# Kernel tuning notes

Measured on AMD Instinct MI355X. Metric: run time of the kernel, lower is better.

## Reference

```python
import jax, jax.numpy as jnp
import numpy as np

DIMS = [1024, 2048, 2048, 51]
B, P = 16, 1024


def setup_inputs() -> dict:
    key = jax.random.key(0)
    ks = jax.random.split(key, 1 + 2 * (len(DIMS) - 1))
    inp = {
        "num_pairs": P,
        "classifier_input": jax.random.normal(ks[0], (B, P, DIMS[0]), dtype=jnp.float32),
        "num_batches": B,
    }
    # Linear params, PyTorch-style: W[out, in], b[out]
    for li in range(len(DIMS) - 1):
        fan_in = DIMS[li]
        bound = 1.0 / np.sqrt(fan_in)
        inp[f"W{li}"] = jax.random.uniform(ks[1 + 2 * li], (DIMS[li + 1], fan_in), minval=-bound, maxval=bound, dtype=jnp.float32)
        inp[f"b{li}"] = jax.random.uniform(ks[2 + 2 * li], (DIMS[li + 1],), minval=-bound, maxval=bound, dtype=jnp.float32)
    return inp


def reference(num_pairs, classifier_input, num_batches, W0, b0, W1, b1, W2, b2):
    # Batched MLP over all (num_batches * num_pairs) vectors at once.
    # Original loops per (b, i); math is identical. dropout p=0.0 -> identity.
    x = classifier_input  # [B, P, d_in]
    x = jax.nn.relu(jnp.einsum("bpd,hd->bph", x, W0) + b0)
    x = jax.nn.relu(jnp.einsum("bpd,hd->bph", x, W1) + b1)
    out = jnp.einsum("bpd,od->bpo", x, W2) + b2  # [B, P, n_classes]
    return out
```

## Files before the change

### kernel.cpp

```cpp
#include <hip/hip_runtime.h>
#include <hip/hip_bf16.h>
#include <stdint.h>

typedef __attribute__((ext_vector_type(8))) short short8;
typedef __attribute__((ext_vector_type(8))) uint16_t ushort8;
typedef __attribute__((ext_vector_type(4))) float floatx4;

#define TK 64


__device__ __forceinline__ uint16_t f2bf_bits(float f) {
    uint32_t u = __builtin_bit_cast(uint32_t, f);
    u += 0x7FFFu + ((u >> 16) & 1u);
    return (uint16_t)(u >> 16);
}

__device__ __forceinline__ void async_copy16(const void* g, void* l) {
    auto gp = (const __attribute__((address_space(1))) uint32_t*)(uintptr_t)g;
    auto lp = (__attribute__((address_space(3))) uint32_t*)(uint32_t)(uintptr_t)l;
    __builtin_amdgcn_global_load_lds(gp, lp, 16, 0, 0);
}


__global__ void cvt8(const float* __restrict__ src, uint16_t* __restrict__ dst, int n) {
    int i = (blockIdx.x * 256 + threadIdx.x) * 8;
    if (i >= n) return;
    floatx4 a = *(const floatx4*)(src + i);
    floatx4 b = *(const floatx4*)(src + i + 4);
    ushort8 o;
#pragma unroll
    for (int k = 0; k < 4; k++) {
        o[k]     = f2bf_bits(a[k]);
        o[k + 4] = f2bf_bits(b[k]);
    }
    *(ushort8*)(dst + i) = o;
}

__global__ void cvt_pad_w2(const float* __restrict__ src, uint16_t* __restrict__ dst) {
    int i = (blockIdx.x * 256 + threadIdx.x) * 8;
    int row = i >> 11;
    ushort8 o;
    if (row < 51) {
        floatx4 a = *(const floatx4*)(src + i);
        floatx4 b = *(const floatx4*)(src + i + 4);
#pragma unroll
        for (int k = 0; k < 4; k++) {
            o[k]     = f2bf_bits(a[k]);
            o[k + 4] = f2bf_bits(b[k]);
        }
    } else {
#pragma unroll
        for (int k = 0; k < 8; k++) o[k] = 0;
    }
    *(ushort8*)(dst + i) = o;
}


template <int MI, int NJ, bool RELU, bool OUTF32>
__global__ __launch_bounds__(256, 2)
void gemm_bt(const uint16_t* __restrict__ A,
             const uint16_t* __restrict__ W,
             const float* __restrict__ bias,
             void* __restrict__ out,
             int M, int N, int K, int ldc, int nstore)
{
    constexpr int TMv = MI * 32;
    constexpr int TNv = NJ * 32;
    constexpr int ACH = TMv / 32;
    constexpr int BCH = TNv / 32;

    __shared__ alignas(16) uint16_t sA[TMv * TK];
    __shared__ alignas(16) uint16_t sB[TNv * TK];

    const int tid  = threadIdx.x;
    const int wave = tid >> 6;
    const int lane = tid & 63;

    const int f   = blockIdx.x;
    const int xcd = f & 7;
    const int loc = f >> 3;
    const int per = (int)gridDim.x >> 3;
    const int nt  = N / TNv;
    const int n_t = loc % nt;
    const int m_t = xcd * (per / nt) + loc / nt;
    const int n0 = n_t * TNv;
    const int m0 = m_t * TMv;

    floatx4 acc[MI][NJ];
    const floatx4 zero = {0.f, 0.f, 0.f, 0.f};
#pragma unroll
    for (int i = 0; i < MI; i++)
#pragma unroll
        for (int j = 0; j < NJ; j++) acc[i][j] = zero;

    const int wr = (wave >> 1) * MI * 16;
    const int wc = (wave & 1) * NJ * 16;

    const int sr   = lane >> 3;
    const int scol = ((lane & 7) ^ sr) * 8;

    const uint16_t* ap[ACH];
    const uint16_t* bp[BCH];
#pragma unroll
    for (int t = 0; t < ACH; t++)
        ap[t] = A + (size_t)(m0 + (wave + 4 * t) * 8 + sr) * K + scol;
#pragma unroll
    for (int t = 0; t < BCH; t++)
        bp[t] = W + (size_t)(n0 + (wave + 4 * t) * 8 + sr) * K + scol;

    const int fm = lane & 15;
    const int fr = fm & 7;
    const int kgb = lane >> 4;

    const int niter = K / TK;
    for (int it = 0; it < niter; it++) {
#pragma unroll
        for (int t = 0; t < ACH; t++) {
            async_copy16(ap[t], sA + (wave + 4 * t) * 512);
            ap[t] += TK;
        }
#pragma unroll
        for (int t = 0; t < BCH; t++) {
            async_copy16(bp[t], sB + (wave + 4 * t) * 512);
            bp[t] += TK;
        }
        __syncthreads();

#pragma unroll
        for (int kk = 0; kk < 2; kk++) {
            const int slot = ((kgb + 4 * kk) ^ fr) * 8;
            short8 af[MI], bfr[NJ];
#pragma unroll
            for (int i = 0; i < MI; i++)
                af[i] = *(const short8*)(sA + (wr + i * 16 + fm) * TK + slot);
#pragma unroll
            for (int j = 0; j < NJ; j++)
                bfr[j] = *(const short8*)(sB + (wc + j * 16 + fm) * TK + slot);
#pragma unroll
            for (int i = 0; i < MI; i++)
#pragma unroll
                for (int j = 0; j < NJ; j++)
                    acc[i][j] = __builtin_amdgcn_mfma_f32_16x16x32_bf16(af[i], bfr[j], acc[i][j], 0, 0, 0);
        }
        __syncthreads();
    }

    const int cr = (lane >> 4) * 4;
    const int cc = lane & 15;
#pragma unroll
    for (int i = 0; i < MI; i++) {
        const int gmb = m0 + wr + i * 16 + cr;
#pragma unroll
        for (int j = 0; j < NJ; j++) {
            const int gn = n0 + wc + j * 16 + cc;
            if (gn < nstore) {
                const float bv = bias[gn];
#pragma unroll
                for (int r = 0; r < 4; r++) {
                    float v = acc[i][j][r] + bv;
                    if (RELU) v = fmaxf(v, 0.f);
                    const size_t idx = (size_t)(gmb + r) * ldc + gn;
                    if (OUTF32) ((float*)out)[idx] = v;
                    else        ((uint16_t*)out)[idx] = f2bf_bits(v);
                }
            }
        }
    }
}


extern "C" void kernel_launch(void* const* d_in, const int* in_sizes, int n_in,
                              void* d_out, int out_size, void* d_ws, size_t ws_size,
                              hipStream_t stream) {
    (void)in_sizes; (void)n_in; (void)out_size; (void)ws_size;
    const float* X  = (const float*)d_in[1];
    const float* W0 = (const float*)d_in[3];
    const float* b0 = (const float*)d_in[4];
    const float* W1 = (const float*)d_in[5];
    const float* b1 = (const float*)d_in[6];
    const float* W2 = (const float*)d_in[7];
    const float* b2 = (const float*)d_in[8];

    const int M = 16384;

    char* w = (char*)d_ws;
    uint16_t* X0  = (uint16_t*)w; w += (size_t)M * 1024 * 2;
    uint16_t* X1  = (uint16_t*)w; w += (size_t)M * 2048 * 2;
    uint16_t* X2  = (uint16_t*)w; w += (size_t)M * 2048 * 2;
    uint16_t* W0b = (uint16_t*)w; w += (size_t)2048 * 1024 * 2;
    uint16_t* W1b = (uint16_t*)w; w += (size_t)2048 * 2048 * 2;
    uint16_t* W2b = (uint16_t*)w; w += (size_t)64 * 2048 * 2;

    cvt8<<<M * 1024 / 8 / 256, 256, 0, stream>>>(X, X0, M * 1024);
    cvt8<<<2048 * 1024 / 8 / 256, 256, 0, stream>>>(W0, W0b, 2048 * 1024);
    cvt8<<<2048 * 2048 / 8 / 256, 256, 0, stream>>>(W1, W1b, 2048 * 2048);
    cvt_pad_w2<<<64 * 2048 / 8 / 256, 256, 0, stream>>>(W2, W2b);

    gemm_bt<4, 8, true, false><<<dim3((M / 128) * (2048 / 256)), 256, 0, stream>>>(
        X0, W0b, b0, X1, M, 2048, 1024, 2048, 2048);
    gemm_bt<4, 8, true, false><<<dim3((M / 128) * (2048 / 256)), 256, 0, stream>>>(
        X1, W1b, b1, X2, M, 2048, 2048, 2048, 2048);
    gemm_bt<1, 2, false, true><<<dim3(M / 32), 256, 0, stream>>>(
        X2, W2b, b2, d_out, M, 64, 2048, 51, 51);
}
```

Measured before the change: 347.6 us.

## Double-buffer GEMM K-tiles, split-K the final layer with atomics, fuse weight conversions

The GEMM kernel now uses two shared-memory buffers with a K tile of 32. The next tile's async global-to-LDS load is issued before computing on the current one, so memory latency overlaps with MFMA work. The swizzle pattern is adjusted for the narrower tile. The last layer (N=64) is split along K into 8 chunks with 128-row tiles and accumulates into a bias-initialized output via float atomicAdd, to expose more parallelism. The three weight-conversion kernels are merged into one launch. The risks are more barriers per K step, atomic contention, and the non-deterministic order of the float sums.

Measured after the change: 401.3 us. 1.15x slower.

```diff
diff --git a/kernel.cpp b/kernel.cpp
--- a/kernel.cpp
+++ b/kernel.cpp
@@ -6,7 +6,7 @@
 typedef __attribute__((ext_vector_type(8))) uint16_t ushort8;
 typedef __attribute__((ext_vector_type(4))) float floatx4;
 
-#define TK 64
+#define TK 32
 
 
 __device__ __forceinline__ uint16_t f2bf_bits(float f) {
@@ -21,70 +21,82 @@
     __builtin_amdgcn_global_load_lds(gp, lp, 16, 0, 0);
 }
 
+__device__ __forceinline__ void cvt8_one(const float* __restrict__ s, uint16_t* __restrict__ d) {
+    floatx4 a = *(const floatx4*)(s);
+    floatx4 b = *(const floatx4*)(s + 4);
+    ushort8 o;
+#pragma unroll
+    for (int k = 0; k < 4; k++) { o[k] = f2bf_bits(a[k]); o[k + 4] = f2bf_bits(b[k]); }
+    *(ushort8*)(d) = o;
+}
+
 
 __global__ void cvt8(const float* __restrict__ src, uint16_t* __restrict__ dst, int n) {
     int i = (blockIdx.x * 256 + threadIdx.x) * 8;
-    if (i >= n) return;
-    floatx4 a = *(const floatx4*)(src + i);
-    floatx4 b = *(const floatx4*)(src + i + 4);
-    ushort8 o;
-#pragma unroll
-    for (int k = 0; k < 4; k++) {
-        o[k]     = f2bf_bits(a[k]);
-        o[k + 4] = f2bf_bits(b[k]);
-    }
-    *(ushort8*)(dst + i) = o;
-}
-
-__global__ void cvt_pad_w2(const float* __restrict__ src, uint16_t* __restrict__ dst) {
+    if (i < n) cvt8_one(src + i, dst + i);
+}
+
+__global__ void cvt_weights(const float* __restrict__ W0, const float* __restrict__ W1,
+                            const float* __restrict__ W2,
+                            uint16_t* __restrict__ o0, uint16_t* __restrict__ o1,
+                            uint16_t* __restrict__ o2) {
     int i = (blockIdx.x * 256 + threadIdx.x) * 8;
-    int row = i >> 11;
-    ushort8 o;
-    if (row < 51) {
-        floatx4 a = *(const floatx4*)(src + i);
-        floatx4 b = *(const floatx4*)(src + i + 4);
-#pragma unroll
-        for (int k = 0; k < 4; k++) {
-            o[k]     = f2bf_bits(a[k]);
-            o[k + 4] = f2bf_bits(b[k]);
-        }
+    if (i < 2097152) {
+        cvt8_one(W0 + i, o0 + i);
+    } else if (i < 2097152 + 4194304) {
+        int j = i - 2097152;
+        cvt8_one(W1 + j, o1 + j);
     } else {
-#pragma unroll
-        for (int k = 0; k < 8; k++) o[k] = 0;
-    }
-    *(ushort8*)(dst + i) = o;
-}
-
-
-template <int MI, int NJ, bool RELU, bool OUTF32>
+        int j = i - 6291456;
+        if (j < 131072) {
+            int row = j >> 11;
+            if (row < 51) cvt8_one(W2 + j, o2 + j);
+            else { ushort8 z = {0,0,0,0,0,0,0,0}; *(ushort8*)(o2 + j) = z; }
+        }
+    }
+}
+
+__global__ void init_bias(const float* __restrict__ b2, float* __restrict__ out, int n) {
+    int i = blockIdx.x * 256 + threadIdx.x;
+    if (i < n) out[i] = b2[i % 51];
+}
+
+
+template <int MI, int NJ, int SPLITK, bool RELU, bool OUTF32, bool ATOMIC>
 __global__ __launch_bounds__(256, 2)
 void gemm_bt(const uint16_t* __restrict__ A,
              const uint16_t* __restrict__ W,
              const float* __restrict__ bias,
              void* __restrict__ out,
-             int M, int N, int K, int ldc, int nstore)
+             int M, int N, int lda, int kspan, int ldc, int nstore)
 {
     constexpr int TMv = MI * 32;
     constexpr int TNv = NJ * 32;
-    constexpr int ACH = TMv / 32;
-    constexpr int BCH = TNv / 32;
-
-    __shared__ alignas(16) uint16_t sA[TMv * TK];
-    __shared__ alignas(16) uint16_t sB[TNv * TK];
+    constexpr int ACH = TMv / 64;
+    constexpr int BCH = TNv / 64;
+
+    __shared__ alignas(16) uint16_t sA[2][TMv * TK];
+    __shared__ alignas(16) uint16_t sB[2][TNv * TK];
 
     const int tid  = threadIdx.x;
     const int wave = tid >> 6;
     const int lane = tid & 63;
 
-    const int f   = blockIdx.x;
-    const int xcd = f & 7;
-    const int loc = f >> 3;
-    const int per = (int)gridDim.x >> 3;
-    const int nt  = N / TNv;
-    const int n_t = loc % nt;
-    const int m_t = xcd * (per / nt) + loc / nt;
-    const int n0 = n_t * TNv;
-    const int m0 = m_t * TMv;
+    const int f = blockIdx.x;
+    int m0, n0, kbeg;
+    if constexpr (SPLITK > 1) {
+        kbeg = (f % SPLITK) * kspan;
+        m0   = (f / SPLITK) * TMv;
+        n0   = 0;
+    } else {
+        kbeg = 0;
+        const int xcd = f & 7;
+        const int loc = f >> 3;
+        const int per = (int)gridDim.x >> 3;
+        const int nt  = N / TNv;
+        n0 = (loc % nt) * TNv;
+        m0 = (xcd * (per / nt) + loc / nt) * TMv;
+    }
 
     floatx4 acc[MI][NJ];
     const floatx4 zero = {0.f, 0.f, 0.f, 0.f};
@@ -96,53 +108,58 @@
     const int wr = (wave >> 1) * MI * 16;
     const int wc = (wave & 1) * NJ * 16;
 
-    const int sr   = lane >> 3;
-    const int scol = ((lane & 7) ^ sr) * 8;
+    const int sr   = lane >> 2;
+    const int scol = ((lane & 3) ^ ((lane >> 3) & 3)) * 8;
 
     const uint16_t* ap[ACH];
     const uint16_t* bp[BCH];
 #pragma unroll
     for (int t = 0; t < ACH; t++)
-        ap[t] = A + (size_t)(m0 + (wave + 4 * t) * 8 + sr) * K + scol;
+        ap[t] = A + (size_t)(m0 + (wave + 4 * t) * 16 + sr) * lda + kbeg + scol;
 #pragma unroll
     for (int t = 0; t < BCH; t++)
-        bp[t] = W + (size_t)(n0 + (wave + 4 * t) * 8 + sr) * K + scol;
+        bp[t] = W + (size_t)(n0 + (wave + 4 * t) * 16 + sr) * lda + kbeg + scol;
+
+    auto prefetch = [&](int buf) {
+#pragma unroll
+        for (int t = 0; t < ACH; t++) {
+            async_copy16(ap[t], &sA[buf][(wave + 4 * t) * 512]);
+            ap[t] += TK;
+        }
+#pragma unroll
+        for (int t = 0; t < BCH; t++) {
+            async_copy16(bp[t], &sB[buf][(wave + 4 * t) * 512]);
+            bp[t] += TK;
+        }
+    };
 
     const int fm = lane & 15;
-    const int fr = fm & 7;
-    const int kgb = lane >> 4;
-
-    const int niter = K / TK;
-    for (int it = 0; it < niter; it++) {
-#pragma unroll
-        for (int t = 0; t < ACH; t++) {
-            async_copy16(ap[t], sA + (wave + 4 * t) * 512);
-            ap[t] += TK;
-        }
-#pragma unroll
-        for (int t = 0; t < BCH; t++) {
-            async_copy16(bp[t], sB + (wave + 4 * t) * 512);
-            bp[t] += TK;
-        }
+    const int slot = ((lane >> 4) ^ ((fm >> 1) & 3)) * 8;
+
+    auto compute = [&](int buf) {
+        short8 af[MI], bfr[NJ];
+#pragma unroll
+        for (int i = 0; i < MI; i++)
+            af[i] = *(const short8*)(&sA[buf][(wr + i * 16 + fm) * TK + slot]);
+#pragma unroll
+        for (int j = 0; j < NJ; j++)
+            bfr[j] = *(const short8*)(&sB[buf][(wc + j * 16 + fm) * TK + slot]);
+#pragma unroll
+        for (int i = 0; i < MI; i++)
+#pragma unroll
+            for (int j = 0; j < NJ; j++)
+                acc[i][j] = __builtin_amdgcn_mfma_f32_16x16x32_bf16(af[i], bfr[j], acc[i][j], 0, 0, 0);
+    };
+
+    const int niter = kspan / TK;
+    prefetch(0);
+    for (int it = 0; it < niter; it += 2) {
         __syncthreads();
-
-#pragma unroll
-        for (int kk = 0; kk < 2; kk++) {
-            const int slot = ((kgb + 4 * kk) ^ fr) * 8;
-            short8 af[MI], bfr[NJ];
-#pragma unroll
-            for (int i = 0; i < MI; i++)
-                af[i] = *(const short8*)(sA + (wr + i * 16 + fm) * TK + slot);
-#pragma unroll
-            for (int j = 0; j < NJ; j++)
-                bfr[j] = *(const short8*)(sB + (wc + j * 16 + fm) * TK + slot);
-#pragma unroll
-            for (int i = 0; i < MI; i++)
-#pragma unroll
-                for (int j = 0; j < NJ; j++)
-                    acc[i][j] = __builtin_amdgcn_mfma_f32_16x16x32_bf16(af[i], bfr[j], acc[i][j], 0, 0, 0);
-        }
+        if (it + 1 < niter) prefetch(1);
+        compute(0);
         __syncthreads();
+        if (it + 2 < niter) prefetch(0);
+        compute(1);
     }
 
     const int cr = (lane >> 4) * 4;
@@ -154,14 +171,16 @@
         for (int j = 0; j < NJ; j++) {
             const int gn = n0 + wc + j * 16 + cc;
             if (gn < nstore) {
-                const float bv = bias[gn];
+                float bv = 0.f;
+                if constexpr (!ATOMIC) bv = bias[gn];
 #pragma unroll
                 for (int r = 0; r < 4; r++) {
                     float v = acc[i][j][r] + bv;
                     if (RELU) v = fmaxf(v, 0.f);
                     const size_t idx = (size_t)(gmb + r) * ldc + gn;
-                    if (OUTF32) ((float*)out)[idx] = v;
-                    else        ((uint16_t*)out)[idx] = f2bf_bits(v);
+                    if constexpr (ATOMIC)      atomicAdd(&((float*)out)[idx], v);
+                    else if constexpr (OUTF32) ((float*)out)[idx] = v;
+                    else                       ((uint16_t*)out)[idx] = f2bf_bits(v);
                 }
             }
         }
@@ -191,15 +210,15 @@
     uint16_t* W1b = (uint16_t*)w; w += (size_t)2048 * 2048 * 2;
     uint16_t* W2b = (uint16_t*)w; w += (size_t)64 * 2048 * 2;
 
+    init_bias<<<(M * 51 + 255) / 256, 256, 0, stream>>>(b2, (float*)d_out, M * 51);
     cvt8<<<M * 1024 / 8 / 256, 256, 0, stream>>>(X, X0, M * 1024);
-    cvt8<<<2048 * 1024 / 8 / 256, 256, 0, stream>>>(W0, W0b, 2048 * 1024);
-    cvt8<<<2048 * 2048 / 8 / 256, 256, 0, stream>>>(W1, W1b, 2048 * 2048);
-    cvt_pad_w2<<<64 * 2048 / 8 / 256, 256, 0, stream>>>(W2, W2b);
-
-    gemm_bt<4, 8, true, false><<<dim3((M / 128) * (2048 / 256)), 256, 0, stream>>>(
-        X0, W0b, b0, X1, M, 2048, 1024, 2048, 2048);
-    gemm_bt<4, 8, true, false><<<dim3((M / 128) * (2048 / 256)), 256, 0, stream>>>(
-        X1, W1b, b1, X2, M, 2048, 2048, 2048, 2048);
-    gemm_bt<1, 2, false, true><<<dim3(M / 32), 256, 0, stream>>>(
-        X2, W2b, b2, d_out, M, 64, 2048, 51, 51);
-}
+    cvt_weights<<<(2097152 + 4194304 + 131072) / 8 / 256, 256, 0, stream>>>(
+        W0, W1, W2, W0b, W1b, W2b);
+
+    gemm_bt<4, 8, 1, true, false, false><<<dim3((M / 128) * (2048 / 256)), 256, 0, stream>>>(
+        X0, W0b, b0, X1, M, 2048, 1024, 1024, 2048, 2048);
+    gemm_bt<4, 8, 1, true, false, false><<<dim3((M / 128) * (2048 / 256)), 256, 0, stream>>>(
+        X1, W1b, b1, X2, M, 2048, 2048, 2048, 2048, 2048);
+    gemm_bt<4, 2, 8, false, true, true><<<dim3((M / 128) * 8), 256, 0, stream>>>(
+        X2, W2b, nullptr, d_out, M, 64, 2048, 256, 51, 51);
+}
```
